# Kernel optimization log

Measured on AMD Instinct MI355X. Metric: run time of the kernel, lower is better.

The kernel has to match this reference:

```python
import jax, jax.numpy as jnp
import numpy as np

UNITS = 14336
IN_FEATURES = 4096
PACKED = IN_FEATURES // 4  # 4 ternary values (2 bits each) per byte
CLIP_VAL = 100.0

# 2-bit crumb -> ternary value lookup: 0 -> 0, 1 -> +1, 2 -> -1, 3 -> 0
_TERNARY_LUT = jnp.array([0.0, 1.0, -1.0, 0.0], dtype=jnp.float32)


def _unpack_ternary(pw):
    """pw: [U, P] int (byte values 0..255) -> dense ternary float W [U, 4*P].
    Little-endian crumbs within each byte (shifts 0,2,4,6)."""
    crumbs = jnp.stack([(pw >> (2 * i)) & 3 for i in range(4)], axis=-1)  # [U, P, 4]
    crumbs = crumbs.reshape(pw.shape[0], -1)  # [U, 4*P]
    return _TERNARY_LUT[crumbs][:, :IN_FEATURES]  # [U, IN]


def setup_inputs() -> dict:
    key = jax.random.key(0)
    k1, k2, k3, k4 = jax.random.split(key, 4)
    x = jax.random.normal(k1, (32, IN_FEATURES), dtype=jnp.float32)
    # packed ternary weights, one uint8-valued byte per 4 ternary weights
    pw = jax.random.randint(k2, (UNITS, PACKED), 0, 256, dtype=jnp.int32)
    scale = 1.0 + 0.02 * jax.random.normal(k3, (UNITS,), dtype=jnp.float32)
    bias = 0.01 * jax.random.normal(k4, (UNITS,), dtype=jnp.float32)
    return {"x": x, "pw": pw, "scale": scale, "bias": bias}


def reference(x, pw, scale, bias):
    # dense ternary weight [UNITS, IN]; kernel target would fuse this unpack into the GEMM
    W = _unpack_ternary(pw)
    y = jnp.einsum('bd,ud->bu', x, W)  # [B, UNITS]
    y = y * scale + bias               # per-unit affine dequant
    return jnp.clip(y, -CLIP_VAL, CLIP_VAL)
```

## Files before the change

### kernel.cpp

```cpp
#include <hip/hip_runtime.h>

#define UNITS 14336
#define IN_F 4096
#define PACKED 1024
#define CLIP_VAL 100.0f

typedef unsigned int uint32;
typedef unsigned short ushort16;

using bf16x8 = __attribute__((ext_vector_type(8))) short;
using f32x4  = __attribute__((ext_vector_type(4))) float;

__device__ inline unsigned short f2bf(float f) {
    uint32 u = __float_as_uint(f);
    u += 0x7FFFu + ((u >> 16) & 1u);
    return (unsigned short)(u >> 16);
}

__global__ __launch_bounds__(256) void convert_x_kernel(
    const float* __restrict__ x, uint4* __restrict__ ws) {
    int t = blockIdx.x * 256 + threadIdx.x;
    int s = t >> 7;
    int h = (t >> 6) & 1;
    int lane = t & 63;
    int b = h * 16 + (lane & 15);
    int k = s * 32 + ((lane >> 4) << 3);
    const float4* src = (const float4*)(x + b * IN_F + k);
    float4 lo = src[0];
    float4 hi = src[1];
    uint4 o;
    o.x = (uint32)f2bf(lo.x) | ((uint32)f2bf(lo.y) << 16);
    o.y = (uint32)f2bf(lo.z) | ((uint32)f2bf(lo.w) << 16);
    o.z = (uint32)f2bf(hi.x) | ((uint32)f2bf(hi.y) << 16);
    o.w = (uint32)f2bf(hi.z) | ((uint32)f2bf(hi.w) << 16);
    ws[t] = o;
}

__device__ inline void unpack_byte(int v, uint32& r0, uint32& r1) {
    uint32 t0 = ((uint32)v & 3u) | (((uint32)v & 0xCu) << 14);
    uint32 t1 = (((uint32)v >> 4) & 3u) | (((uint32)v & 0xC0u) << 10);
    uint32 s0 = t0 >> 1;
    uint32 s1 = t1 >> 1;
    uint32 nz0 = (t0 ^ s0) & 0x00010001u;
    uint32 nz1 = (t1 ^ s1) & 0x00010001u;
    r0 = nz0 * 0x3F80u + ((s0 & 0x00010001u) << 15);
    r1 = nz1 * 0x3F80u + ((s1 & 0x00010001u) << 15);
}

__device__ inline float clipf(float y) {
    return fminf(fmaxf(y, -CLIP_VAL), CLIP_VAL);
}

__global__ __launch_bounds__(256) void ternary_mm_kernel(
    const uint4* __restrict__ xw,
    const int*   __restrict__ pw,
    const float* __restrict__ scale,
    const float* __restrict__ bias,
    float*       __restrict__ out) {
    __shared__ float4 red[4][128];

    const int tid  = threadIdx.x;
    const int wid  = tid >> 6;
    const int lane = tid & 63;
    const int u0   = blockIdx.x << 4;
    const int urow = u0 + (lane & 15);
    const int q    = lane >> 4;

    f32x4 acc0 = {0.f, 0.f, 0.f, 0.f};
    f32x4 acc1 = {0.f, 0.f, 0.f, 0.f};

    const int s_begin = wid << 5;
    const int*   pwbase = pw + urow * PACKED + (q << 1) + (s_begin << 3);
    const uint4* xbase  = xw + (s_begin << 1) * 64 + lane;

    #pragma unroll 4
    for (int i = 0; i < 32; ++i) {
        uint4 a0u = xbase[i * 128];
        uint4 a1u = xbase[i * 128 + 64];
        int2 w2 = *(const int2*)(pwbase + i * 8);

        uint4 bu;
        unpack_byte(w2.x, bu.x, bu.y);
        unpack_byte(w2.y, bu.z, bu.w);
        bf16x8 bfrag = __builtin_bit_cast(bf16x8, bu);

        acc0 = __builtin_amdgcn_mfma_f32_16x16x32_bf16(
            __builtin_bit_cast(bf16x8, a0u), bfrag, acc0, 0, 0, 0);
        acc1 = __builtin_amdgcn_mfma_f32_16x16x32_bf16(
            __builtin_bit_cast(bf16x8, a1u), bfrag, acc1, 0, 0, 0);
    }

    red[wid][lane]      = make_float4(acc0[0], acc0[1], acc0[2], acc0[3]);
    red[wid][64 + lane] = make_float4(acc1[0], acc1[1], acc1[2], acc1[3]);
    __syncthreads();

    if (tid < 128) {
        const int f = tid >> 6;
        const int l = tid & 63;
        float4 v0 = red[0][f * 64 + l];
        float4 v1 = red[1][f * 64 + l];
        float4 v2 = red[2][f * 64 + l];
        float4 v3 = red[3][f * 64 + l];
        float vx = v0.x + v1.x + v2.x + v3.x;
        float vy = v0.y + v1.y + v2.y + v3.y;
        float vz = v0.z + v1.z + v2.z + v3.z;
        float vw = v0.w + v1.w + v2.w + v3.w;

        const int u  = u0 + (l & 15);
        const int b0 = f * 16 + ((l >> 4) << 2);
        const float sc = scale[u];
        const float bi = bias[u];
        float* o = out + (size_t)b0 * UNITS + u;
        o[0 * UNITS] = clipf(vx * sc + bi);
        o[1 * UNITS] = clipf(vy * sc + bi);
        o[2 * UNITS] = clipf(vz * sc + bi);
        o[3 * UNITS] = clipf(vw * sc + bi);
    }
}

extern "C" void kernel_launch(void* const* d_in, const int* in_sizes, int n_in,
                              void* d_out, int out_size, void* d_ws, size_t ws_size,
                              hipStream_t stream) {
    const float* x     = (const float*)d_in[0];
    const int*   pw    = (const int*)d_in[1];
    const float* scale = (const float*)d_in[2];
    const float* bias  = (const float*)d_in[3];
    float* out = (float*)d_out;

    uint4* xw = (uint4*)d_ws;

    convert_x_kernel<<<64, 256, 0, stream>>>(x, xw);
    ternary_mm_kernel<<<UNITS / 16, 256, 0, stream>>>(xw, pw, scale, bias, out);
}
```

Before: 112.7 us.

## Widen block to 32 units with 8 waves splitting K and reuse x fragments

Each block now covers 32 output units with 512 threads. The 8 waves split the K dimension into 16-step chunks, and each wave reuses the same x fragments for two weight tiles, giving 4 MFMAs per iteration. This halves the number of x-fragment loads per weight byte and the block count. In exchange the LDS reduction grows to 8 partial sums, and with 448 blocks on 256 CUs the work may not balance evenly. The kernel is likely bound by streaming pw at 4 bytes per int, so the gain may be limited.

```diff
diff --git a/kernel.cpp b/kernel.cpp
--- a/kernel.cpp
+++ b/kernel.cpp
@@ -6,7 +6,6 @@
 #define CLIP_VAL 100.0f
 
 typedef unsigned int uint32;
-typedef unsigned short ushort16;
 
 using bf16x8 = __attribute__((ext_vector_type(8))) short;
 using f32x4  = __attribute__((ext_vector_type(4))) float;
@@ -51,70 +50,80 @@
     return fminf(fmaxf(y, -CLIP_VAL), CLIP_VAL);
 }
 
-__global__ __launch_bounds__(256) void ternary_mm_kernel(
+__global__ __launch_bounds__(512) void ternary_mm_kernel(
     const uint4* __restrict__ xw,
     const int*   __restrict__ pw,
     const float* __restrict__ scale,
     const float* __restrict__ bias,
     float*       __restrict__ out) {
-    __shared__ float4 red[4][128];
+    __shared__ f32x4 red[8][4][64];
 
     const int tid  = threadIdx.x;
     const int wid  = tid >> 6;
     const int lane = tid & 63;
-    const int u0   = blockIdx.x << 4;
-    const int urow = u0 + (lane & 15);
     const int q    = lane >> 4;
+    const int n    = lane & 15;
+    const int u0   = blockIdx.x << 5;
 
-    f32x4 acc0 = {0.f, 0.f, 0.f, 0.f};
-    f32x4 acc1 = {0.f, 0.f, 0.f, 0.f};
+    f32x4 acc00 = {0.f,0.f,0.f,0.f};
+    f32x4 acc10 = {0.f,0.f,0.f,0.f};
+    f32x4 acc01 = {0.f,0.f,0.f,0.f};
+    f32x4 acc11 = {0.f,0.f,0.f,0.f};
 
-    const int s_begin = wid << 5;
-    const int*   pwbase = pw + urow * PACKED + (q << 1) + (s_begin << 3);
-    const uint4* xbase  = xw + (s_begin << 1) * 64 + lane;
+    const int s_begin = wid << 4;
+    const int* pA = pw + (size_t)(u0 + n)      * PACKED + (q << 1) + (s_begin << 3);
+    const int* pB = pw + (size_t)(u0 + 16 + n) * PACKED + (q << 1) + (s_begin << 3);
+    const uint4* xb = xw + (s_begin << 7) + lane;
 
     #pragma unroll 4
-    for (int i = 0; i < 32; ++i) {
-        uint4 a0u = xbase[i * 128];
-        uint4 a1u = xbase[i * 128 + 64];
-        int2 w2 = *(const int2*)(pwbase + i * 8);
+    for (int i = 0; i < 16; ++i) {
+        uint4 a0u = xb[i * 128];
+        uint4 a1u = xb[i * 128 + 64];
+        int2 wA = *(const int2*)(pA + i * 8);
+        int2 wB = *(const int2*)(pB + i * 8);
 
-        uint4 bu;
-        unpack_byte(w2.x, bu.x, bu.y);
-        unpack_byte(w2.y, bu.z, bu.w);
-        bf16x8 bfrag = __builtin_bit_cast(bf16x8, bu);
+        uint4 bA, bB;
+        unpack_byte(wA.x, bA.x, bA.y);
+        unpack_byte(wA.y, bA.z, bA.w);
+        unpack_byte(wB.x, bB.x, bB.y);
+        unpack_byte(wB.y, bB.z, bB.w);
+        bf16x8 fA = __builtin_bit_cast(bf16x8, bA);
+        bf16x8 fB = __builtin_bit_cast(bf16x8, bB);
+        bf16x8 x0 = __builtin_bit_cast(bf16x8, a0u);
+        bf16x8 x1 = __builtin_bit_cast(bf16x8, a1u);
 
-        acc0 = __builtin_amdgcn_mfma_f32_16x16x32_bf16(
-            __builtin_bit_cast(bf16x8, a0u), bfrag, acc0, 0, 0, 0);
-        acc1 = __builtin_amdgcn_mfma_f32_16x16x32_bf16(
-            __builtin_bit_cast(bf16x8, a1u), bfrag, acc1, 0, 0, 0);
+        acc00 = __builtin_amdgcn_mfma_f32_16x16x32_bf16(x0, fA, acc00, 0, 0, 0);
+        acc10 = __builtin_amdgcn_mfma_f32_16x16x32_bf16(x1, fA, acc10, 0, 0, 0);
+        acc01 = __builtin_amdgcn_mfma_f32_16x16x32_bf16(x0, fB, acc01, 0, 0, 0);
+        acc11 = __builtin_amdgcn_mfma_f32_16x16x32_bf16(x1, fB, acc11, 0, 0, 0);
     }
 
-    red[wid][lane]      = make_float4(acc0[0], acc0[1], acc0[2], acc0[3]);
-    red[wid][64 + lane] = make_float4(acc1[0], acc1[1], acc1[2], acc1[3]);
+    red[wid][0][lane] = acc00;
+    red[wid][1][lane] = acc10;
+    red[wid][2][lane] = acc01;
+    red[wid][3][lane] = acc11;
     __syncthreads();
 
-    if (tid < 128) {
+    if (tid < 256) {
         const int f = tid >> 6;
         const int l = tid & 63;
-        float4 v0 = red[0][f * 64 + l];
-        float4 v1 = red[1][f * 64 + l];
-        float4 v2 = red[2][f * 64 + l];
-        float4 v3 = red[3][f * 64 + l];
-        float vx = v0.x + v1.x + v2.x + v3.x;
-        float vy = v0.y + v1.y + v2.y + v3.y;
-        float vz = v0.z + v1.z + v2.z + v3.z;
-        float vw = v0.w + v1.w + v2.w + v3.w;
-
-        const int u  = u0 + (l & 15);
-        const int b0 = f * 16 + ((l >> 4) << 2);
+        f32x4 s = red[0][f][l];
+        #pragma unroll
+        for (int w = 1; w < 8; ++w) {
+            f32x4 v = red[w][f][l];
+            s[0] += v[0]; s[1] += v[1]; s[2] += v[2]; s[3] += v[3];
+        }
+        const int g = f >> 1;
+        const int h = f & 1;
+        const int u  = u0 + g * 16 + (l & 15);
+        const int b0 = h * 16 + ((l >> 4) << 2);
         const float sc = scale[u];
         const float bi = bias[u];
         float* o = out + (size_t)b0 * UNITS + u;
-        o[0 * UNITS] = clipf(vx * sc + bi);
-        o[1 * UNITS] = clipf(vy * sc + bi);
-        o[2 * UNITS] = clipf(vz * sc + bi);
-        o[3 * UNITS] = clipf(vw * sc + bi);
+        o[0 * UNITS] = clipf(s[0] * sc + bi);
+        o[1 * UNITS] = clipf(s[1] * sc + bi);
+        o[2 * UNITS] = clipf(s[2] * sc + bi);
+        o[3 * UNITS] = clipf(s[3] * sc + bi);
     }
 }
 
@@ -130,5 +139,5 @@
     uint4* xw = (uint4*)d_ws;
 
     convert_x_kernel<<<64, 256, 0, stream>>>(x, xw);
-    ternary_mm_kernel<<<UNITS / 16, 256, 0, stream>>>(xw, pw, scale, bias, out);
+    ternary_mm_kernel<<<UNITS / 32, 512, 0, stream>>>(xw, pw, scale, bias, out);
 }
```

After: 110.6 us. No clear change (-1.9%).
